# Optimization experiments

Measured on AMD Instinct MI355X. Metric: run time of the kernel, lower is better.

The kernel has to match this reference:

```python
import jax, jax.numpy as jnp
import numpy as np

B, LQ, LKV, D = 2, 256, 256, 512
STD = 0.02


def setup_inputs() -> dict:
    key0 = jax.random.key(0)
    ks = jax.random.split(key0, 10)
    return {
        "key": jax.random.normal(ks[0], (B, LKV, D), jnp.float32),
        "query": jax.random.normal(ks[1], (B, LQ, D), jnp.float32),
        "value": jax.random.normal(ks[2], (B, LKV, D), jnp.float32),
        "mask": jax.random.bernoulli(ks[3], 0.9, (B, LQ, LKV)),
        # projection weights (torch Linear: y = x @ W.T + b), init std=0.02, bias=0
        "W_k": STD * jax.random.normal(ks[4], (D, D), jnp.float32),
        "b_k": jnp.zeros((D,), jnp.float32),
        "W_v": STD * jax.random.normal(ks[5], (D, D), jnp.float32),
        "b_v": jnp.zeros((D,), jnp.float32),
        "W_q": STD * jax.random.normal(ks[6], (D, D), jnp.float32),
        "b_q": jnp.zeros((D,), jnp.float32),
        # additive attention: linear_concat (2D->D) and linear_logit (D->1)
        "W_c": STD * jax.random.normal(ks[7], (D, 2 * D), jnp.float32),
        "b_c": jnp.zeros((D,), jnp.float32),
        "W_l": STD * jax.random.normal(ks[8], (1, D), jnp.float32),
        "b_l": jnp.zeros((1,), jnp.float32),
    }


def reference(key, query, value, mask, W_k, b_k, W_v, b_v, W_q, b_q, W_c, b_c, W_l, b_l):
    d = key.shape[-1]
    k = key @ W_k.T + b_k                       # [B, Lkv, D]
    v = value @ W_v.T + b_v                     # [B, Lkv, D] (computed but unused, as in original)
    q = (query @ W_q.T + b_q) / jnp.sqrt(jnp.asarray(d, key.dtype))  # [B, Lq, D]

    # linear_concat on cat([q, k]) == q @ Wc[:, :D].T + k @ Wc[:, D:].T + b_c
    a_q = q @ W_c[:, :d].T                      # [B, Lq, D]
    a_k = k @ W_c[:, d:].T                      # [B, Lkv, D]
    combined = jnp.tanh(a_q[:, :, None, :] + a_k[:, None, :, :] + b_c)  # [B, Lq, Lkv, D]
    logits = jnp.einsum("bqkd,d->bqk", combined, W_l[0]) + b_l[0]       # [B, Lq, Lkv]

    neg = jnp.logical_not(mask)
    # rows that are fully masked get un-masked (filled with 0) to avoid all -inf
    neg = jnp.logical_and(neg, jnp.logical_not(jnp.all(neg, axis=-1, keepdims=True)))
    logits = jnp.where(neg, -jnp.inf, logits)
    weights = jax.nn.softmax(logits, axis=-1)   # [B, Lq, Lkv]
    return weights
```

## Files before the change

kernel.cpp:

```cpp
#include <hip/hip_runtime.h>


#define LOG2E     1.4426950408889634f
#define TWO_LOG2E 2.8853900817779268f
#define INV_SQRTD 0.04419417382415922f

typedef __attribute__((ext_vector_type(8))) short v8s;
typedef __attribute__((ext_vector_type(4))) float v4f;

#if __has_builtin(__builtin_amdgcn_exp2f)
#define EXP2(x) __builtin_amdgcn_exp2f(x)
#else
#define EXP2(x) exp2f(x)
#endif
#if __has_builtin(__builtin_amdgcn_rcpf)
#define RCP(x) __builtin_amdgcn_rcpf(x)
#else
#define RCP(x) (1.0f/(x))
#endif

__device__ inline unsigned int cvt2bf(float a, float b) {
  unsigned int ua = __float_as_uint(a);
  unsigned int ub = __float_as_uint(b);
  ua = (ua + 0x7FFFu + ((ua >> 16) & 1u)) >> 16;
  ub = (ub + 0x7FFFu + ((ub >> 16) & 1u)) >> 16;
  return ua | (ub << 16);
}

__global__ void detect_mask(const unsigned int* __restrict__ mw, int* __restrict__ flag) {
  unsigned int w = mw[threadIdx.x];
  bool ok = (w == 0u) || (w == 1u) || (w == 0x3F800000u);
  unsigned long long b = __ballot(ok);
  if (threadIdx.x == 0) *flag = (b == 0xFFFFFFFFFFFFFFFFull) ? 0 : 1;
}

__global__ __launch_bounds__(256) void gemm_bt(
    const float* __restrict__ A0, const float* __restrict__ W0, const float* __restrict__ b0,
    float s0, float* __restrict__ o0, int mode0, int ldw0,
    const float* __restrict__ A1, const float* __restrict__ W1, const float* __restrict__ b1,
    float s1, float* __restrict__ o1, int mode1, int ldw1)
{
  const int z = blockIdx.z;
  const float* A    = z ? A1 : A0;
  const float* W    = z ? W1 : W0;
  const float* bias = z ? b1 : b0;
  const float scale = z ? s1 : s0;
  float* out        = z ? o1 : o0;
  const int mode    = z ? mode1 : mode0;
  const int ldw     = z ? ldw1 : ldw0;

  const int m0 = blockIdx.x * 32;
  const int n0 = blockIdx.y * 64;
  const int tid = threadIdx.x;
  const int lane = tid & 63;
  const int wv = tid >> 6;

  __shared__ unsigned char smem[12288];

  const int ar  = tid >> 3;
  const int akg = tid & 7;
  const int br  = tid >> 2;
  const int bq  = tid & 3;

  const int fr = lane & 15;
  const int fk = (lane >> 4) * 16;

  v4f acc0 = {0.f, 0.f, 0.f, 0.f};
  v4f acc1 = {0.f, 0.f, 0.f, 0.f};

  for (int kt = 0; kt < 8; ++kt) {
    const int k0 = kt * 64;
    const float* ap = A + (m0 + ar) * 512 + k0 + akg * 8;
    float4 av0 = *(const float4*)(ap);
    float4 av1 = *(const float4*)(ap + 4);
    const float* bp = W + (n0 + br) * ldw + k0 + bq * 16;
    float4 bv0 = *(const float4*)(bp);
    float4 bv1 = *(const float4*)(bp + 4);
    float4 bv2 = *(const float4*)(bp + 8);
    float4 bv3 = *(const float4*)(bp + 12);

    __syncthreads();
    {
      int addr = (ar * 128 + akg * 16) ^ ((ar & 7) << 4);
      *(uint4*)(smem + addr) = make_uint4(cvt2bf(av0.x, av0.y), cvt2bf(av0.z, av0.w),
                                          cvt2bf(av1.x, av1.y), cvt2bf(av1.z, av1.w));
    }
    {
      int base = br * 128 + bq * 32;
      int addr  = 4096 + ((base)      ^ ((br & 7) << 4));
      int addr2 = 4096 + ((base + 16) ^ ((br & 7) << 4));
      *(uint4*)(smem + addr)  = make_uint4(cvt2bf(bv0.x, bv0.y), cvt2bf(bv0.z, bv0.w),
                                           cvt2bf(bv1.x, bv1.y), cvt2bf(bv1.z, bv1.w));
      *(uint4*)(smem + addr2) = make_uint4(cvt2bf(bv2.x, bv2.y), cvt2bf(bv2.z, bv2.w),
                                           cvt2bf(bv3.x, bv3.y), cvt2bf(bv3.z, bv3.w));
    }
    __syncthreads();

#pragma unroll
    for (int ks = 0; ks < 2; ++ks) {
      const int kb = ks * 64 + fk;
      const int rowb = wv * 16 + fr;
      int ra0 = ((fr)        * 128 + kb) ^ ((fr & 7) << 4);
      int ra1 = ((fr | 16)   * 128 + kb) ^ ((fr & 7) << 4);
      int rb  = 4096 + ((rowb * 128 + kb) ^ ((rowb & 7) << 4));
      v8s a0 = *(const v8s*)(smem + ra0);
      v8s a1 = *(const v8s*)(smem + ra1);
      v8s b  = *(const v8s*)(smem + rb);
      acc0 = __builtin_amdgcn_mfma_f32_16x16x32_bf16(a0, b, acc0, 0, 0, 0);
      acc1 = __builtin_amdgcn_mfma_f32_16x16x32_bf16(a1, b, acc1, 0, 0, 0);
    }
  }

  const int n = n0 + wv * 16 + (lane & 15);
  const int mbase = m0 + (lane >> 4) * 4;
  const float bn = bias ? bias[n] : 0.f;
#pragma unroll
  for (int r = 0; r < 4; ++r) {
    int m  = mbase + r;
    int m2 = m + 16;
    float v0 = (acc0[r] + bn) * scale;
    float v1 = (acc1[r] + bn) * scale;
    if (mode == 0) {
      out[m * 512 + n]  = v0;
      out[m2 * 512 + n] = v1;
    } else {
      out[(m  >> 8) * 131072 + (n >> 2) * 1024 + (m  & 255) * 4 + (n & 3)] = v0;
      out[(m2 >> 8) * 131072 + (n >> 2) * 1024 + (m2 & 255) * 4 + (n & 3)] = v1;
    }
  }
}

__global__ __launch_bounds__(256) void attn_main(
    const float* __restrict__ c2, const float* __restrict__ ak4,
    const void* __restrict__ maskp, const float* __restrict__ Wl,
    const int* __restrict__ flagp, float* __restrict__ out)
{
  const int bx = blockIdx.x;
  const int j  = threadIdx.x;

  __shared__ float2 cw[512];
  __shared__ float red[8];

  for (int dd = j; dd < 512; dd += 256)
    cw[dd] = make_float2(c2[bx * 512 + dd], -2.f * Wl[dd]);
  __syncthreads();

  const float* ak = ak4 + (bx >> 8) * 131072 + j * 4;
  float a0 = 0.f, a1 = 0.f, a2 = 0.f, a3 = 0.f;
#pragma unroll 8
  for (int db = 0; db < 128; ++db) {
    float4 v = *(const float4*)(ak + db * 1024);
    float2 p0 = cw[db * 4 + 0], p1 = cw[db * 4 + 1];
    float2 p2 = cw[db * 4 + 2], p3 = cw[db * 4 + 3];
    a0 += p0.y * RCP(EXP2(p0.x + v.x) + 1.f);
    a1 += p1.y * RCP(EXP2(p1.x + v.y) + 1.f);
    a2 += p2.y * RCP(EXP2(p2.x + v.z) + 1.f);
    a3 += p3.y * RCP(EXP2(p3.x + v.w) + 1.f);
  }
  float l = (a0 + a1) + (a2 + a3);

  const int midx = bx * 256 + j;
  int mv;
  if (*flagp) mv = ((const unsigned char*)maskp)[midx];
  else        mv = ((const int*)maskp)[midx];
  const bool msk = (mv != 0);
  const int any = __syncthreads_or(msk ? 1 : 0);
  const bool use = msk || (any == 0);

  float lm = use ? l : -3.0e38f;
  float wmax = lm;
#pragma unroll
  for (int o = 32; o > 0; o >>= 1) wmax = fmaxf(wmax, __shfl_xor(wmax, o));
  const int wid = j >> 6;
  if ((j & 63) == 0) red[wid] = wmax;
  __syncthreads();
  const float M = fmaxf(fmaxf(red[0], red[1]), fmaxf(red[2], red[3]));

  float p = use ? EXP2((l - M) * LOG2E) : 0.f;
  float s = p;
#pragma unroll
  for (int o = 32; o > 0; o >>= 1) s += __shfl_xor(s, o);
  if ((j & 63) == 0) red[4 + wid] = s;
  __syncthreads();
  const float S = (red[4] + red[5]) + (red[6] + red[7]);

  out[midx] = p * RCP(S);
}

extern "C" void kernel_launch(void* const* d_in, const int* in_sizes, int n_in,
                              void* d_out, int out_size, void* d_ws, size_t ws_size,
                              hipStream_t stream) {
  const float* key   = (const float*)d_in[0];
  const float* query = (const float*)d_in[1];
  const void*  mask  = d_in[3];
  const float* W_k   = (const float*)d_in[4];
  const float* b_k   = (const float*)d_in[5];
  const float* W_q   = (const float*)d_in[8];
  const float* b_q   = (const float*)d_in[9];
  const float* W_c   = (const float*)d_in[10];
  const float* b_c   = (const float*)d_in[11];
  const float* W_l   = (const float*)d_in[12];

  float* ws  = (float*)d_ws;
  float* q2  = ws;
  float* k2  = ws + 262144;
  float* c2  = ws + 524288;
  float* ak4 = ws + 786432;
  int* flag  = (int*)(ws + 1048576);

  detect_mask<<<1, 64, 0, stream>>>((const unsigned int*)mask, flag);

  dim3 g(16, 8, 2);
  gemm_bt<<<g, 256, 0, stream>>>(query, W_q, b_q, INV_SQRTD, q2, 0, 512,
                                 key,   W_k, b_k, 1.0f,      k2, 0, 512);
  gemm_bt<<<g, 256, 0, stream>>>(q2, W_c,       b_c,     TWO_LOG2E, c2,  0, 1024,
                                 k2, W_c + 512, nullptr, TWO_LOG2E, ak4, 1, 1024);

  attn_main<<<512, 256, 0, stream>>>(c2, ak4, mask, W_l, flag, (float*)d_out);
}
```

Measured before the change: 133.3 us.

## Fuse projection GEMMs, precompute exponentials, and drop softmax max pass

The two projection GEMM launches become one kernel. It keeps the first projection in LDS as bf16 and feeds it straight into the W_c projection, recomputing that first projection for each of the two output halves. The exponentials exp(2x) of both additive terms are computed once in that kernel, so the attention loop computes tanh-based terms with an fma and a reciprocal instead of exp2+add+rcp per element. The mask-format detection moves into the attention kernel, removing a launch. The softmax max-reduction is dropped because logits are bounded by the tanh. The trade-offs are less parallelism in the 64-block projection kernel, weight fragments loaded from global memory without LDS reuse, and possible overflow or inf*0 edge cases in the exp product.

```diff
diff --git a/kernel.cpp b/kernel.cpp
--- a/kernel.cpp
+++ b/kernel.cpp
@@ -1,4 +1,5 @@
 #include <hip/hip_runtime.h>
+#include <hip/hip_bf16.h>
 
 
 #define LOG2E     1.4426950408889634f
@@ -19,170 +20,187 @@
 #define RCP(x) (1.0f/(x))
 #endif
 
-__device__ inline unsigned int cvt2bf(float a, float b) {
-  unsigned int ua = __float_as_uint(a);
-  unsigned int ub = __float_as_uint(b);
-  ua = (ua + 0x7FFFu + ((ua >> 16) & 1u)) >> 16;
-  ub = (ub + 0x7FFFu + ((ub >> 16) & 1u)) >> 16;
-  return ua | (ub << 16);
-}
-
-__global__ void detect_mask(const unsigned int* __restrict__ mw, int* __restrict__ flag) {
-  unsigned int w = mw[threadIdx.x];
-  bool ok = (w == 0u) || (w == 1u) || (w == 0x3F800000u);
-  unsigned long long b = __ballot(ok);
-  if (threadIdx.x == 0) *flag = (b == 0xFFFFFFFFFFFFFFFFull) ? 0 : 1;
-}
-
-__global__ __launch_bounds__(256) void gemm_bt(
-    const float* __restrict__ A0, const float* __restrict__ W0, const float* __restrict__ b0,
-    float s0, float* __restrict__ o0, int mode0, int ldw0,
-    const float* __restrict__ A1, const float* __restrict__ W1, const float* __restrict__ b1,
-    float s1, float* __restrict__ o1, int mode1, int ldw1)
+__device__ inline unsigned bfpair(float a, float b) {
+  __hip_bfloat162 h = __float22bfloat162_rn(make_float2(a, b));
+  return *reinterpret_cast<unsigned*>(&h);
+}
+__device__ inline v8s pack8(float4 a, float4 b) {
+  union { unsigned u[4]; v8s v; } r;
+  r.u[0] = bfpair(a.x, a.y); r.u[1] = bfpair(a.z, a.w);
+  r.u[2] = bfpair(b.x, b.y); r.u[3] = bfpair(b.z, b.w);
+  return r.v;
+}
+
+__global__ __launch_bounds__(256) void fused_proj(
+    const float* __restrict__ query, const float* __restrict__ key,
+    const float* __restrict__ Wq, const float* __restrict__ bq,
+    const float* __restrict__ Wk, const float* __restrict__ bk,
+    const float* __restrict__ Wc, const float* __restrict__ bc,
+    float* __restrict__ E, float* __restrict__ G)
 {
-  const int z = blockIdx.z;
-  const float* A    = z ? A1 : A0;
-  const float* W    = z ? W1 : W0;
-  const float* bias = z ? b1 : b0;
-  const float scale = z ? s1 : s0;
-  float* out        = z ? o1 : o0;
-  const int mode    = z ? mode1 : mode0;
-  const int ldw     = z ? ldw1 : ldw0;
-
-  const int m0 = blockIdx.x * 32;
-  const int n0 = blockIdx.y * 64;
+  const int mb = blockIdx.x;
+  const int h  = blockIdx.y;
+  const int c  = blockIdx.z;
   const int tid = threadIdx.x;
   const int lane = tid & 63;
-  const int wv = tid >> 6;
-
-  __shared__ unsigned char smem[12288];
-
-  const int ar  = tid >> 3;
-  const int akg = tid & 7;
-  const int br  = tid >> 2;
-  const int bq  = tid & 3;
-
-  const int fr = lane & 15;
-  const int fk = (lane >> 4) * 16;
-
-  v4f acc0 = {0.f, 0.f, 0.f, 0.f};
-  v4f acc1 = {0.f, 0.f, 0.f, 0.f};
-
-  for (int kt = 0; kt < 8; ++kt) {
-    const int k0 = kt * 64;
-    const float* ap = A + (m0 + ar) * 512 + k0 + akg * 8;
-    float4 av0 = *(const float4*)(ap);
-    float4 av1 = *(const float4*)(ap + 4);
-    const float* bp = W + (n0 + br) * ldw + k0 + bq * 16;
-    float4 bv0 = *(const float4*)(bp);
-    float4 bv1 = *(const float4*)(bp + 4);
-    float4 bv2 = *(const float4*)(bp + 8);
-    float4 bv3 = *(const float4*)(bp + 12);
-
-    __syncthreads();
-    {
-      int addr = (ar * 128 + akg * 16) ^ ((ar & 7) << 4);
-      *(uint4*)(smem + addr) = make_uint4(cvt2bf(av0.x, av0.y), cvt2bf(av0.z, av0.w),
-                                          cvt2bf(av1.x, av1.y), cvt2bf(av1.z, av1.w));
-    }
-    {
-      int base = br * 128 + bq * 32;
-      int addr  = 4096 + ((base)      ^ ((br & 7) << 4));
-      int addr2 = 4096 + ((base + 16) ^ ((br & 7) << 4));
-      *(uint4*)(smem + addr)  = make_uint4(cvt2bf(bv0.x, bv0.y), cvt2bf(bv0.z, bv0.w),
-                                           cvt2bf(bv1.x, bv1.y), cvt2bf(bv1.z, bv1.w));
-      *(uint4*)(smem + addr2) = make_uint4(cvt2bf(bv2.x, bv2.y), cvt2bf(bv2.z, bv2.w),
-                                           cvt2bf(bv3.x, bv3.y), cvt2bf(bv3.z, bv3.w));
-    }
-    __syncthreads();
-
-#pragma unroll
-    for (int ks = 0; ks < 2; ++ks) {
-      const int kb = ks * 64 + fk;
-      const int rowb = wv * 16 + fr;
-      int ra0 = ((fr)        * 128 + kb) ^ ((fr & 7) << 4);
-      int ra1 = ((fr | 16)   * 128 + kb) ^ ((fr & 7) << 4);
-      int rb  = 4096 + ((rowb * 128 + kb) ^ ((rowb & 7) << 4));
-      v8s a0 = *(const v8s*)(smem + ra0);
-      v8s a1 = *(const v8s*)(smem + ra1);
-      v8s b  = *(const v8s*)(smem + rb);
-      acc0 = __builtin_amdgcn_mfma_f32_16x16x32_bf16(a0, b, acc0, 0, 0, 0);
-      acc1 = __builtin_amdgcn_mfma_f32_16x16x32_bf16(a1, b, acc1, 0, 0, 0);
-    }
-  }
-
-  const int n = n0 + wv * 16 + (lane & 15);
-  const int mbase = m0 + (lane >> 4) * 4;
-  const float bn = bias ? bias[n] : 0.f;
-#pragma unroll
-  for (int r = 0; r < 4; ++r) {
-    int m  = mbase + r;
-    int m2 = m + 16;
-    float v0 = (acc0[r] + bn) * scale;
-    float v1 = (acc1[r] + bn) * scale;
-    if (mode == 0) {
-      out[m * 512 + n]  = v0;
-      out[m2 * 512 + n] = v1;
-    } else {
-      out[(m  >> 8) * 131072 + (n >> 2) * 1024 + (m  & 255) * 4 + (n & 3)] = v0;
-      out[(m2 >> 8) * 131072 + (n >> 2) * 1024 + (m2 & 255) * 4 + (n & 3)] = v1;
-    }
-  }
-}
-
-__global__ __launch_bounds__(256) void attn_main(
-    const float* __restrict__ c2, const float* __restrict__ ak4,
+  const int w = tid >> 6;
+
+  const float* A  = c ? key : query;
+  const float* W1 = c ? Wk : Wq;
+  const float* b1 = c ? bk : bq;
+  const float  s1 = c ? 1.0f : INV_SQRTD;
+  const float* W2 = Wc + (c ? 512 : 0);
+
+  __shared__ __align__(16) unsigned char q2s[32 * 1024];
+
+  const int fr  = lane & 15;
+  const int fko = (lane >> 4) * 8;
+  const int m0  = mb * 32;
+
+  v4f acc[2][8];
+#pragma unroll
+  for (int mt = 0; mt < 2; ++mt)
+#pragma unroll
+    for (int nt = 0; nt < 8; ++nt) acc[mt][nt] = (v4f){0.f, 0.f, 0.f, 0.f};
+
+  const float* arow0 = A + (m0 + fr) * 512 + fko;
+  const float* arow1 = arow0 + 16 * 512;
+  const float* brow  = W1 + (w * 128 + fr) * 512 + fko;
+
+  for (int kt = 0; kt < 16; ++kt) {
+    const int k0 = kt * 32;
+    float4 a00 = *(const float4*)(arow0 + k0);
+    float4 a01 = *(const float4*)(arow0 + k0 + 4);
+    float4 a10 = *(const float4*)(arow1 + k0);
+    float4 a11 = *(const float4*)(arow1 + k0 + 4);
+    v8s am0 = pack8(a00, a01);
+    v8s am1 = pack8(a10, a11);
+#pragma unroll
+    for (int nt = 0; nt < 8; ++nt) {
+      const float* bp = brow + nt * (16 * 512) + k0;
+      float4 b0 = *(const float4*)(bp);
+      float4 b1v = *(const float4*)(bp + 4);
+      v8s bf = pack8(b0, b1v);
+      acc[0][nt] = __builtin_amdgcn_mfma_f32_16x16x32_bf16(am0, bf, acc[0][nt], 0, 0, 0);
+      acc[1][nt] = __builtin_amdgcn_mfma_f32_16x16x32_bf16(am1, bf, acc[1][nt], 0, 0, 0);
+    }
+  }
+
+  {
+    const int rbase = (lane >> 4) * 4;
+#pragma unroll
+    for (int nt = 0; nt < 8; ++nt) {
+      const int n1 = w * 128 + nt * 16 + fr;
+      const float bb = b1[n1];
+#pragma unroll
+      for (int mt = 0; mt < 2; ++mt) {
+#pragma unroll
+        for (int r = 0; r < 4; ++r) {
+          const int row = mt * 16 + rbase + r;
+          const float v = (acc[mt][nt][r] + bb) * s1;
+          const int addr = (row * 1024 + n1 * 2) ^ ((row & 7) << 4);
+          *(__hip_bfloat16*)(q2s + addr) = __float2bfloat16(v);
+        }
+      }
+    }
+  }
+  __syncthreads();
+
+  v4f acc2[2][4];
+#pragma unroll
+  for (int mt = 0; mt < 2; ++mt)
+#pragma unroll
+    for (int nt = 0; nt < 4; ++nt) acc2[mt][nt] = (v4f){0.f, 0.f, 0.f, 0.f};
+
+  const float* w2row = W2 + (h * 256 + w * 64 + fr) * 1024 + fko;
+  const int a0r = fr, a1r = fr + 16;
+
+  for (int kt = 0; kt < 16; ++kt) {
+    const int kb = kt * 64 + fko * 2;
+    v8s am0 = *(const v8s*)(q2s + ((a0r * 1024 + kb) ^ ((a0r & 7) << 4)));
+    v8s am1 = *(const v8s*)(q2s + ((a1r * 1024 + kb) ^ ((a1r & 7) << 4)));
+    const int k0 = kt * 32;
+#pragma unroll
+    for (int nt = 0; nt < 4; ++nt) {
+      const float* bp = w2row + nt * (16 * 1024) + k0;
+      float4 b0 = *(const float4*)(bp);
+      float4 b1v = *(const float4*)(bp + 4);
+      v8s bf = pack8(b0, b1v);
+      acc2[0][nt] = __builtin_amdgcn_mfma_f32_16x16x32_bf16(am0, bf, acc2[0][nt], 0, 0, 0);
+      acc2[1][nt] = __builtin_amdgcn_mfma_f32_16x16x32_bf16(am1, bf, acc2[1][nt], 0, 0, 0);
+    }
+  }
+
+  {
+    const int rbase = (lane >> 4) * 4;
+#pragma unroll
+    for (int nt = 0; nt < 4; ++nt) {
+      const int n2 = h * 256 + w * 64 + nt * 16 + fr;
+      const float bb = c ? 0.f : bc[n2];
+#pragma unroll
+      for (int mt = 0; mt < 2; ++mt) {
+#pragma unroll
+        for (int r = 0; r < 4; ++r) {
+          const int m = m0 + mt * 16 + rbase + r;
+          const float v = EXP2(TWO_LOG2E * (acc2[mt][nt][r] + bb));
+          if (c == 0) E[m * 512 + n2] = v;
+          else G[(m >> 8) * 131072 + (n2 >> 2) * 1024 + (m & 255) * 4 + (n2 & 3)] = v;
+        }
+      }
+    }
+  }
+}
+
+__global__ __launch_bounds__(256) void attn_sm(
+    const float* __restrict__ E, const float* __restrict__ G,
     const void* __restrict__ maskp, const float* __restrict__ Wl,
-    const int* __restrict__ flagp, float* __restrict__ out)
+    float* __restrict__ out)
 {
   const int bx = blockIdx.x;
   const int j  = threadIdx.x;
 
   __shared__ float2 cw[512];
-  __shared__ float red[8];
-
+  __shared__ float red[4];
+  __shared__ int sflag;
+
+  if (j < 64) {
+    unsigned wrd = ((const unsigned*)maskp)[j];
+    bool ok = (wrd == 0u) | (wrd == 1u) | (wrd == 0x3F800000u);
+    unsigned long long bl = __ballot(ok);
+    if (j == 0) sflag = (~bl == 0ull) ? 0 : 1;
+  }
   for (int dd = j; dd < 512; dd += 256)
-    cw[dd] = make_float2(c2[bx * 512 + dd], -2.f * Wl[dd]);
+    cw[dd] = make_float2(E[bx * 512 + dd], -2.f * Wl[dd]);
   __syncthreads();
 
-  const float* ak = ak4 + (bx >> 8) * 131072 + j * 4;
+  const float* g = G + (bx >> 8) * 131072 + j * 4;
   float a0 = 0.f, a1 = 0.f, a2 = 0.f, a3 = 0.f;
 #pragma unroll 8
   for (int db = 0; db < 128; ++db) {
-    float4 v = *(const float4*)(ak + db * 1024);
+    float4 v = *(const float4*)(g + db * 1024);
     float2 p0 = cw[db * 4 + 0], p1 = cw[db * 4 + 1];
     float2 p2 = cw[db * 4 + 2], p3 = cw[db * 4 + 3];
-    a0 += p0.y * RCP(EXP2(p0.x + v.x) + 1.f);
-    a1 += p1.y * RCP(EXP2(p1.x + v.y) + 1.f);
-    a2 += p2.y * RCP(EXP2(p2.x + v.z) + 1.f);
-    a3 += p3.y * RCP(EXP2(p3.x + v.w) + 1.f);
+    a0 += p0.y * RCP(__builtin_fmaf(p0.x, v.x, 1.f));
+    a1 += p1.y * RCP(__builtin_fmaf(p1.x, v.y, 1.f));
+    a2 += p2.y * RCP(__builtin_fmaf(p2.x, v.z, 1.f));
+    a3 += p3.y * RCP(__builtin_fmaf(p3.x, v.w, 1.f));
   }
   float l = (a0 + a1) + (a2 + a3);
 
   const int midx = bx * 256 + j;
-  int mv;
-  if (*flagp) mv = ((const unsigned char*)maskp)[midx];
-  else        mv = ((const int*)maskp)[midx];
+  const int mv = sflag ? (int)((const unsigned char*)maskp)[midx]
+                       : ((const int*)maskp)[midx];
   const bool msk = (mv != 0);
   const int any = __syncthreads_or(msk ? 1 : 0);
   const bool use = msk || (any == 0);
 
-  float lm = use ? l : -3.0e38f;
-  float wmax = lm;
-#pragma unroll
-  for (int o = 32; o > 0; o >>= 1) wmax = fmaxf(wmax, __shfl_xor(wmax, o));
-  const int wid = j >> 6;
-  if ((j & 63) == 0) red[wid] = wmax;
+  float p = use ? EXP2(l * LOG2E) : 0.f;
+  float s = p;
+#pragma unroll
+  for (int o = 32; o > 0; o >>= 1) s += __shfl_xor(s, o);
+  if ((j & 63) == 0) red[j >> 6] = s;
   __syncthreads();
-  const float M = fmaxf(fmaxf(red[0], red[1]), fmaxf(red[2], red[3]));
-
-  float p = use ? EXP2((l - M) * LOG2E) : 0.f;
-  float s = p;
-#pragma unroll
-  for (int o = 32; o > 0; o >>= 1) s += __shfl_xor(s, o);
-  if ((j & 63) == 0) red[4 + wid] = s;
-  __syncthreads();
-  const float S = (red[4] + red[5]) + (red[6] + red[7]);
+  const float S = (red[0] + red[1]) + (red[2] + red[3]);
 
   out[midx] = p * RCP(S);
 }
@@ -201,20 +219,11 @@
   const float* b_c   = (const float*)d_in[11];
   const float* W_l   = (const float*)d_in[12];
 
-  float* ws  = (float*)d_ws;
-  float* q2  = ws;
-  float* k2  = ws + 262144;
-  float* c2  = ws + 524288;
-  float* ak4 = ws + 786432;
-  int* flag  = (int*)(ws + 1048576);
-
-  detect_mask<<<1, 64, 0, stream>>>((const unsigned int*)mask, flag);
-
-  dim3 g(16, 8, 2);
-  gemm_bt<<<g, 256, 0, stream>>>(query, W_q, b_q, INV_SQRTD, q2, 0, 512,
-                                 key,   W_k, b_k, 1.0f,      k2, 0, 512);
-  gemm_bt<<<g, 256, 0, stream>>>(q2, W_c,       b_c,     TWO_LOG2E, c2,  0, 1024,
-                                 k2, W_c + 512, nullptr, TWO_LOG2E, ak4, 1, 1024);
-
-  attn_main<<<512, 256, 0, stream>>>(c2, ak4, mask, W_l, flag, (float*)d_out);
-}
+  float* ws = (float*)d_ws;
+  float* E  = ws;
+  float* G  = ws + 262144;
+
+  fused_proj<<<dim3(16, 2, 2), 256, 0, stream>>>(query, key, W_q, b_q, W_k, b_k,
+                                                 W_c, b_c, E, G);
+  attn_sm<<<512, 256, 0, stream>>>(E, G, mask, W_l, (float*)d_out);
+}
```

Result: slower. 155.9 us (+17.0%).

## Factor tanh exponent into GEMM epilogues, drop softmax max pass and mask-detect kernel

Applied to the files above, without the earlier changes.

The second GEMM now applies exp2 in its epilogue, so the inner loop of the attention kernel computes exp2(a+b) as a product E*G with one FMA instead of an exp per element. The softmax max-reduction pass is removed on the assumption that logits are bounded (|logit| ≤ 2·sum|W_l|), and the mask-format detection is folded into the attention kernel, removing one launch. The GEMM also prefetches the next K tile into registers before the MFMA loop. The risks are overflow or underflow in the exp products, since the exponent magnitude depends on the input data, and the loss of max-subtraction stability in the softmax.

```diff
diff --git a/kernel.cpp b/kernel.cpp
--- a/kernel.cpp
+++ b/kernel.cpp
@@ -1,4 +1,5 @@
 #include <hip/hip_runtime.h>
+#include <hip/hip_bf16.h>
 
 
 #define LOG2E     1.4426950408889634f
@@ -19,26 +20,19 @@
 #define RCP(x) (1.0f/(x))
 #endif
 
-__device__ inline unsigned int cvt2bf(float a, float b) {
-  unsigned int ua = __float_as_uint(a);
-  unsigned int ub = __float_as_uint(b);
+__device__ inline unsigned cvt2bf(float a, float b) {
+  unsigned ua = __float_as_uint(a);
+  unsigned ub = __float_as_uint(b);
   ua = (ua + 0x7FFFu + ((ua >> 16) & 1u)) >> 16;
   ub = (ub + 0x7FFFu + ((ub >> 16) & 1u)) >> 16;
   return ua | (ub << 16);
 }
 
-__global__ void detect_mask(const unsigned int* __restrict__ mw, int* __restrict__ flag) {
-  unsigned int w = mw[threadIdx.x];
-  bool ok = (w == 0u) || (w == 1u) || (w == 0x3F800000u);
-  unsigned long long b = __ballot(ok);
-  if (threadIdx.x == 0) *flag = (b == 0xFFFFFFFFFFFFFFFFull) ? 0 : 1;
-}
-
 __global__ __launch_bounds__(256) void gemm_bt(
     const float* __restrict__ A0, const float* __restrict__ W0, const float* __restrict__ b0,
-    float s0, float* __restrict__ o0, int mode0, int ldw0,
+    float s0, float* __restrict__ o0, int mode0, int ldw0, int em0,
     const float* __restrict__ A1, const float* __restrict__ W1, const float* __restrict__ b1,
-    float s1, float* __restrict__ o1, int mode1, int ldw1)
+    float s1, float* __restrict__ o1, int mode1, int ldw1, int em1)
 {
   const int z = blockIdx.z;
   const float* A    = z ? A1 : A0;
@@ -48,6 +42,7 @@
   float* out        = z ? o1 : o0;
   const int mode    = z ? mode1 : mode0;
   const int ldw     = z ? ldw1 : ldw0;
+  const int em      = z ? em1 : em0;
 
   const int m0 = blockIdx.x * 32;
   const int n0 = blockIdx.y * 64;
@@ -55,7 +50,7 @@
   const int lane = tid & 63;
   const int wv = tid >> 6;
 
-  __shared__ unsigned char smem[12288];
+  __shared__ __align__(16) unsigned char smem[12288];
 
   const int ar  = tid >> 3;
   const int akg = tid & 7;
@@ -68,40 +63,48 @@
   v4f acc0 = {0.f, 0.f, 0.f, 0.f};
   v4f acc1 = {0.f, 0.f, 0.f, 0.f};
 
+  const float* apb = A + (m0 + ar) * 512 + akg * 8;
+  const float* bpb = W + (n0 + br) * ldw + bq * 16;
+
+  float4 av0 = *(const float4*)(apb);
+  float4 av1 = *(const float4*)(apb + 4);
+  float4 bv0 = *(const float4*)(bpb);
+  float4 bv1 = *(const float4*)(bpb + 4);
+  float4 bv2 = *(const float4*)(bpb + 8);
+  float4 bv3 = *(const float4*)(bpb + 12);
+
   for (int kt = 0; kt < 8; ++kt) {
-    const int k0 = kt * 64;
-    const float* ap = A + (m0 + ar) * 512 + k0 + akg * 8;
-    float4 av0 = *(const float4*)(ap);
-    float4 av1 = *(const float4*)(ap + 4);
-    const float* bp = W + (n0 + br) * ldw + k0 + bq * 16;
-    float4 bv0 = *(const float4*)(bp);
-    float4 bv1 = *(const float4*)(bp + 4);
-    float4 bv2 = *(const float4*)(bp + 8);
-    float4 bv3 = *(const float4*)(bp + 12);
-
     __syncthreads();
     {
       int addr = (ar * 128 + akg * 16) ^ ((ar & 7) << 4);
       *(uint4*)(smem + addr) = make_uint4(cvt2bf(av0.x, av0.y), cvt2bf(av0.z, av0.w),
                                           cvt2bf(av1.x, av1.y), cvt2bf(av1.z, av1.w));
-    }
-    {
       int base = br * 128 + bq * 32;
-      int addr  = 4096 + ((base)      ^ ((br & 7) << 4));
-      int addr2 = 4096 + ((base + 16) ^ ((br & 7) << 4));
-      *(uint4*)(smem + addr)  = make_uint4(cvt2bf(bv0.x, bv0.y), cvt2bf(bv0.z, bv0.w),
-                                           cvt2bf(bv1.x, bv1.y), cvt2bf(bv1.z, bv1.w));
-      *(uint4*)(smem + addr2) = make_uint4(cvt2bf(bv2.x, bv2.y), cvt2bf(bv2.z, bv2.w),
-                                           cvt2bf(bv3.x, bv3.y), cvt2bf(bv3.z, bv3.w));
+      int a1 = 4096 + ((base)      ^ ((br & 7) << 4));
+      int a2 = 4096 + ((base + 16) ^ ((br & 7) << 4));
+      *(uint4*)(smem + a1) = make_uint4(cvt2bf(bv0.x, bv0.y), cvt2bf(bv0.z, bv0.w),
+                                        cvt2bf(bv1.x, bv1.y), cvt2bf(bv1.z, bv1.w));
+      *(uint4*)(smem + a2) = make_uint4(cvt2bf(bv2.x, bv2.y), cvt2bf(bv2.z, bv2.w),
+                                        cvt2bf(bv3.x, bv3.y), cvt2bf(bv3.z, bv3.w));
     }
     __syncthreads();
+
+    if (kt < 7) {
+      const int k0 = (kt + 1) * 64;
+      av0 = *(const float4*)(apb + k0);
+      av1 = *(const float4*)(apb + k0 + 4);
+      bv0 = *(const float4*)(bpb + k0);
+      bv1 = *(const float4*)(bpb + k0 + 4);
+      bv2 = *(const float4*)(bpb + k0 + 8);
+      bv3 = *(const float4*)(bpb + k0 + 12);
+    }
 
 #pragma unroll
     for (int ks = 0; ks < 2; ++ks) {
       const int kb = ks * 64 + fk;
       const int rowb = wv * 16 + fr;
-      int ra0 = ((fr)        * 128 + kb) ^ ((fr & 7) << 4);
-      int ra1 = ((fr | 16)   * 128 + kb) ^ ((fr & 7) << 4);
+      int ra0 = ((fr)      * 128 + kb) ^ ((fr & 7) << 4);
+      int ra1 = ((fr | 16) * 128 + kb) ^ ((fr & 7) << 4);
       int rb  = 4096 + ((rowb * 128 + kb) ^ ((rowb & 7) << 4));
       v8s a0 = *(const v8s*)(smem + ra0);
       v8s a1 = *(const v8s*)(smem + ra1);
@@ -120,6 +123,7 @@
     int m2 = m + 16;
     float v0 = (acc0[r] + bn) * scale;
     float v1 = (acc1[r] + bn) * scale;
+    if (em) { v0 = EXP2(v0); v1 = EXP2(v1); }
     if (mode == 0) {
       out[m * 512 + n]  = v0;
       out[m2 * 512 + n] = v1;
@@ -130,59 +134,56 @@
   }
 }
 
-__global__ __launch_bounds__(256) void attn_main(
-    const float* __restrict__ c2, const float* __restrict__ ak4,
+__global__ __launch_bounds__(256) void attn_sm(
+    const float* __restrict__ E, const float* __restrict__ G,
     const void* __restrict__ maskp, const float* __restrict__ Wl,
-    const int* __restrict__ flagp, float* __restrict__ out)
+    float* __restrict__ out)
 {
   const int bx = blockIdx.x;
   const int j  = threadIdx.x;
 
   __shared__ float2 cw[512];
-  __shared__ float red[8];
-
+  __shared__ float red[4];
+  __shared__ int sflag;
+
+  if (j < 64) {
+    unsigned wrd = ((const unsigned*)maskp)[j];
+    bool ok = (wrd == 0u) | (wrd == 1u) | (wrd == 0x3F800000u);
+    unsigned long long bl = __ballot(ok);
+    if (j == 0) sflag = (~bl == 0ull) ? 0 : 1;
+  }
   for (int dd = j; dd < 512; dd += 256)
-    cw[dd] = make_float2(c2[bx * 512 + dd], -2.f * Wl[dd]);
+    cw[dd] = make_float2(E[bx * 512 + dd], -2.f * Wl[dd]);
   __syncthreads();
 
-  const float* ak = ak4 + (bx >> 8) * 131072 + j * 4;
+  const float* g = G + (bx >> 8) * 131072 + j * 4;
   float a0 = 0.f, a1 = 0.f, a2 = 0.f, a3 = 0.f;
 #pragma unroll 8
   for (int db = 0; db < 128; ++db) {
-    float4 v = *(const float4*)(ak + db * 1024);
+    float4 v = *(const float4*)(g + db * 1024);
     float2 p0 = cw[db * 4 + 0], p1 = cw[db * 4 + 1];
     float2 p2 = cw[db * 4 + 2], p3 = cw[db * 4 + 3];
-    a0 += p0.y * RCP(EXP2(p0.x + v.x) + 1.f);
-    a1 += p1.y * RCP(EXP2(p1.x + v.y) + 1.f);
-    a2 += p2.y * RCP(EXP2(p2.x + v.z) + 1.f);
-    a3 += p3.y * RCP(EXP2(p3.x + v.w) + 1.f);
+    a0 += p0.y * RCP(__builtin_fmaf(p0.x, v.x, 1.f));
+    a1 += p1.y * RCP(__builtin_fmaf(p1.x, v.y, 1.f));
+    a2 += p2.y * RCP(__builtin_fmaf(p2.x, v.z, 1.f));
+    a3 += p3.y * RCP(__builtin_fmaf(p3.x, v.w, 1.f));
   }
   float l = (a0 + a1) + (a2 + a3);
 
   const int midx = bx * 256 + j;
-  int mv;
-  if (*flagp) mv = ((const unsigned char*)maskp)[midx];
-  else        mv = ((const int*)maskp)[midx];
+  const int mv = sflag ? (int)((const unsigned char*)maskp)[midx]
+                       : ((const int*)maskp)[midx];
   const bool msk = (mv != 0);
   const int any = __syncthreads_or(msk ? 1 : 0);
   const bool use = msk || (any == 0);
 
-  float lm = use ? l : -3.0e38f;
-  float wmax = lm;
-#pragma unroll
-  for (int o = 32; o > 0; o >>= 1) wmax = fmaxf(wmax, __shfl_xor(wmax, o));
-  const int wid = j >> 6;
-  if ((j & 63) == 0) red[wid] = wmax;
-  __syncthreads();
-  const float M = fmaxf(fmaxf(red[0], red[1]), fmaxf(red[2], red[3]));
-
-  float p = use ? EXP2((l - M) * LOG2E) : 0.f;
+  float p = use ? EXP2(l * LOG2E) : 0.f;
   float s = p;
 #pragma unroll
   for (int o = 32; o > 0; o >>= 1) s += __shfl_xor(s, o);
-  if ((j & 63) == 0) red[4 + wid] = s;
+  if ((j & 63) == 0) red[j >> 6] = s;
   __syncthreads();
-  const float S = (red[4] + red[5]) + (red[6] + red[7]);
+  const float S = (red[0] + red[1]) + (red[2] + red[3]);
 
   out[midx] = p * RCP(S);
 }
@@ -201,20 +202,16 @@
   const float* b_c   = (const float*)d_in[11];
   const float* W_l   = (const float*)d_in[12];
 
-  float* ws  = (float*)d_ws;
-  float* q2  = ws;
-  float* k2  = ws + 262144;
-  float* c2  = ws + 524288;
-  float* ak4 = ws + 786432;
-  int* flag  = (int*)(ws + 1048576);
-
-  detect_mask<<<1, 64, 0, stream>>>((const unsigned int*)mask, flag);
+  float* ws = (float*)d_ws;
+  float* q2 = ws;
+  float* k2 = ws + 262144;
+  float* E  = ws + 524288;
+  float* G  = ws + 786432;
 
   dim3 g(16, 8, 2);
-  gemm_bt<<<g, 256, 0, stream>>>(query, W_q, b_q, INV_SQRTD, q2, 0, 512,
-                                 key,   W_k, b_k, 1.0f,      k2, 0, 512);
-  gemm_bt<<<g, 256, 0, stream>>>(q2, W_c,       b_c,     TWO_LOG2E, c2,  0, 1024,
-                                 k2, W_c + 512, nullptr, TWO_LOG2E, ak4, 1, 1024);
-
-  attn_main<<<512, 256, 0, stream>>>(c2, ak4, mask, W_l, flag, (float*)d_out);
-}
+  gemm_bt<<<g, 256, 0, stream>>>(query, W_q, b_q, INV_SQRTD, q2, 0, 512, 0,
+                                 key,   W_k, b_k, 1.0f,      k2, 0, 512, 0);
+  gemm_bt<<<g, 256, 0, stream>>>(q2, W_c,       b_c,     TWO_LOG2E, E, 0, 1024, 1,
+                                 k2, W_c + 512, nullptr, TWO_LOG2E, G, 1, 1024, 1);
+  attn_sm<<<512, 256, 0, stream>>>(E, G, mask, W_l, (float*)d_out);
+}
```

New measurement: 119.1 us. 1.12x faster.
